# Kernel tuning notes

Hardware: AMD Instinct MI355X
Metric: run time of the kernel (lower is better)

## Reference

```python
import jax, jax.numpy as jnp
import numpy as np

ROWS, COLS, CH = 16, 16, 3
HID, HEADS, BLEN = 512, 8, 128
NUM_POINTS = ROWS * COLS            # 256
SEQ = ROWS * COLS * CH              # 768
NF = 256
L = 6
EPS = 1e-6


def setup_inputs() -> dict:
    key = jax.random.key(0)
    ks = jax.random.split(key, 16)
    w = 0.02  # keep logits in a sane range
    return {
        "X": jax.random.uniform(ks[0], (16, CH, ROWS, COLS), jnp.float32),
        "embed_table": jax.random.normal(ks[1], (NUM_POINTS * CH, HID), jnp.float32) * w,
        "Wq": jax.random.normal(ks[2], (L, HID, HID), jnp.float32) * w,
        "Wk": jax.random.normal(ks[3], (L, HID, HID), jnp.float32) * w,
        "Wv": jax.random.normal(ks[4], (L, HID, HID), jnp.float32) * w,
        "Wo": jax.random.normal(ks[5], (L, HID, HID), jnp.float32) * w,
        "ln1_g": jnp.ones((L, HID), jnp.float32),
        "ln1_b": jnp.zeros((L, HID), jnp.float32),
        "W1": jax.random.normal(ks[6], (L, HID, 4 * HID), jnp.float32) * w,
        "b1": jnp.zeros((L, 4 * HID), jnp.float32),
        "W2": jax.random.normal(ks[7], (L, 4 * HID, HID), jnp.float32) * w,
        "b2": jnp.zeros((L, HID), jnp.float32),
        "ln2_g": jnp.ones((L, HID), jnp.float32),
        "ln2_b": jnp.zeros((L, HID), jnp.float32),
        "proj_W": jax.random.normal(ks[8], (HID * SEQ, NF), jnp.float32) * w,
        "out_ln_g": jnp.ones((NF,), jnp.float32),
        "out_ln_b": jnp.zeros((NF,), jnp.float32),
    }


def _ln(x, g, b):
    m = jnp.mean(x, axis=-1, keepdims=True)
    v = jnp.mean(jnp.square(x - m), axis=-1, keepdims=True)
    return (x - m) * jax.lax.rsqrt(v + EPS) * g + b


def _timing_signal(x4):
    # x4: [B, ROWS, COLS*CH, HID]; 2 spatial dims
    nts = HID // 4
    inv = jnp.exp(jnp.arange(nts, dtype=jnp.float32) * (-np.log(10000.0) / (nts - 1)))
    def sig(length, prepad, postpad):
        pos = jnp.arange(length, dtype=jnp.float32)
        st = pos[:, None] * inv[None, :]
        s = jnp.concatenate([jnp.sin(st), jnp.cos(st)], axis=1)  # [len, 2*nts]
        return jnp.pad(s, ((0, 0), (prepad, postpad)))
    s0 = sig(x4.shape[1], 0, HID - 2 * nts)          # dim 0 (rows)
    s1 = sig(x4.shape[2], 2 * nts, 0)                # dim 1 (cols*ch)
    return x4 + s0[None, :, None, :] + s1[None, None, :, :]


def _local_attn(x, wq, wk, wv, wo):
    B, S, _ = x.shape
    dh = HID // HEADS
    def heads(w):
        return (x @ w).reshape(B, S, HEADS, dh).transpose(0, 2, 1, 3)
    q = heads(wq) * (dh ** -0.5)
    k = heads(wk)
    v = heads(wv)
    nb = S // BLEN  # S is a multiple of BLEN here (768/128=6), so no padding
    neg = jnp.float32(-1e9)
    bias1 = neg * jnp.triu(jnp.ones((BLEN, BLEN), jnp.float32), 1)
    logits1 = jnp.einsum('bhkd,bhqd->bhqk', k[:, :, :BLEN], q[:, :, :BLEN]) + bias1
    first = jax.nn.softmax(logits1, axis=-1) @ v[:, :, :BLEN]  # [B,H,BLEN,dh]
    qb = q.reshape(B, HEADS, nb, BLEN, dh)
    kb = k.reshape(B, HEADS, nb, BLEN, dh)
    vb = v.reshape(B, HEADS, nb, BLEN, dh)
    lk = jnp.concatenate([kb[:, :, :-1], kb[:, :, 1:]], axis=3)  # [B,H,nb-1,2B,dh]
    lv = jnp.concatenate([vb[:, :, :-1], vb[:, :, 1:]], axis=3)
    tq = qb[:, :, 1:]
    bias2 = neg * jnp.triu(jnp.ones((BLEN, 2 * BLEN), jnp.float32), BLEN + 1)
    logits2 = jnp.einsum('bhnkd,bhnqd->bhnqk', lk, tq) + bias2
    tail = jnp.einsum('bhnqk,bhnkd->bhnqd', jax.nn.softmax(logits2, axis=-1), lv)
    tail = tail.reshape(B, HEADS, (nb - 1) * BLEN, dh)
    out = jnp.concatenate([first, tail], axis=2)  # [B,H,S,dh]
    out = out.transpose(0, 2, 1, 3).reshape(B, S, HID)
    return out @ wo


def reference(X, embed_table, Wq, Wk, Wv, Wo, ln1_g, ln1_b, W1, b1, W2, b2,
              ln2_g, ln2_b, proj_W, out_ln_g, out_ln_b):
    B = X.shape[0]
    # [B,C,H,W] -> [B,H,W,C] -> [B,H,W*C]
    x = X.transpose(0, 2, 3, 1).reshape(B, ROWS, COLS * CH)
    idx = (x * (NUM_POINTS - 1)).astype(jnp.int32)
    chan_add = jnp.tile(jnp.arange(CH, dtype=jnp.int32) * NUM_POINTS, COLS)  # [W*C]
    idx = idx + chan_add[None, None, :]
    e = embed_table[idx] * (HID ** 0.5)             # [B,H,W*C,HID]
    # shift_and_pad over flattened spatial dims
    flat = e.reshape(B, SEQ, HID)
    flat = jnp.pad(flat[:, :-1], ((0, 0), (1, 0), (0, 0)))
    e = flat.reshape(B, ROWS, COLS * CH, HID)
    e = _timing_signal(e)
    h = e.reshape(B, SEQ, HID)
    for i in range(L):
        y = _local_attn(h, Wq[i], Wk[i], Wv[i], Wo[i])
        h = _ln(y + h, ln1_g[i], ln1_b[i])
        y = jax.nn.gelu(h @ W1[i] + b1[i], approximate=False) @ W2[i] + b2[i]
        h = _ln(y + h, ln2_g[i], ln2_b[i])
    out = h.reshape(B, SEQ * HID) @ proj_W
    out = jax.nn.gelu(out, approximate=False)
    return _ln(out, out_ln_g, out_ln_b)
```

## Files before the change

### kernel.cpp

```cpp
#include <hip/hip_runtime.h>
#include <cstddef>

typedef __bf16 bf16;
typedef bf16 bf16x4 __attribute__((ext_vector_type(4)));
typedef bf16 bf16x8 __attribute__((ext_vector_type(8)));
typedef float f32x4 __attribute__((ext_vector_type(4)));

#define NLAYER 6
#define HIDD 512
#define SEQL 768
#define NBATCH 16
#define MROWS 12288
#define QKVS 1536

__device__ __forceinline__ void gll16(const void* g, void* l) {
  __builtin_amdgcn_global_load_lds((const __attribute__((address_space(1))) void*)g,
                                   (__attribute__((address_space(3))) void*)l, 16, 0, 0);
}

__device__ __forceinline__ float gelu_f(float v) {
  return 0.5f * v * (1.0f + erff(v * 0.7071067811865475f));
}

#define VMC8 asm volatile("s_waitcnt vmcnt(8)" ::: "memory");
#define VMC4 asm volatile("s_waitcnt vmcnt(4)" ::: "memory");
#define VMC0 asm volatile("s_waitcnt vmcnt(0)" ::: "memory");

__global__ __launch_bounds__(256) void prep(
    const float* __restrict__ X, const float* __restrict__ ET,
    const float* __restrict__ Wq, const float* __restrict__ Wk,
    const float* __restrict__ Wv, const float* __restrict__ Wo,
    const float* __restrict__ W1, const float* __restrict__ W2,
    const float* __restrict__ ln1g, const float* __restrict__ ln1b,
    const float* __restrict__ ln2g, const float* __restrict__ ln2b,
    bf16* __restrict__ Wqkvt, bf16* __restrict__ Wot,
    bf16* __restrict__ W1t, bf16* __restrict__ W2t,
    float* __restrict__ vQg, float* __restrict__ vQb,
    float* __restrict__ vW1g, float* __restrict__ vW1b,
    bf16* __restrict__ Zg2) {
  const int bx = blockIdx.x;
  const int t = threadIdx.x;
  if (bx < 18432) {
    const int l = bx / 3072, idx = bx % 3072;
    const float* src;
    bf16* dst;
    int K, N, kb, nb;
    if (idx < 1024) {
      const int which = idx >> 8, tile = idx & 255;
      nb = (tile & 15) * 32; kb = (tile >> 4) * 32; K = 512; N = 512;
      const float* s4[4] = {Wq, Wk, Wv, Wo};
      src = s4[which] + (size_t)l * 512 * 512;
      dst = (which < 3) ? (Wqkvt + (size_t)l * QKVS * 512 + (size_t)which * 512 * 512)
                        : (Wot + (size_t)l * 512 * 512);
    } else if (idx < 2048) {
      const int local = idx - 1024;
      nb = (local & 63) * 32; kb = (local >> 6) * 32; K = 512; N = 2048;
      src = W1 + (size_t)l * 512 * 2048; dst = W1t + (size_t)l * 512 * 2048;
    } else {
      const int local = idx - 2048;
      nb = (local & 15) * 32; kb = (local >> 4) * 32; K = 2048; N = 512;
      src = W2 + (size_t)l * 2048 * 512; dst = W2t + (size_t)l * 2048 * 512;
    }
    __shared__ float tile[32 * 33];
#pragma unroll
    for (int i = 0; i < 4; ++i) {
      int lin = i * 256 + t, r = lin >> 5, c = lin & 31;
      tile[r * 33 + c] = src[(size_t)(kb + r) * N + nb + c];
    }
    __syncthreads();
#pragma unroll
    for (int i = 0; i < 4; ++i) {
      int lin = i * 256 + t, r = lin >> 5, c = lin & 31;
      dst[(size_t)(nb + r) * K + kb + c] = (bf16)tile[c * 33 + r];
    }
    return;
  }
  if (bx < 18432 + 84) {
    const int i = bx - 18432;
    const int l = i / 14;
    const int c = (i % 14) * 256 + t;
    if (c < 1536) {
      float gv = 0.f, bv = 0.f;
      if (l > 0) {
        const float* gin = ln2g + (l - 1) * 512;
        const float* bin = ln2b + (l - 1) * 512;
        const float* W;
        int cc = c;
        if (c < 512) { W = Wq + (size_t)l * 512 * 512; }
        else if (c < 1024) { W = Wk + (size_t)l * 512 * 512; cc = c - 512; }
        else { W = Wv + (size_t)l * 512 * 512; cc = c - 1024; }
        for (int k = 0; k < 512; ++k) {
          const float w = W[(size_t)k * 512 + cc];
          gv += gin[k] * w;
          bv += bin[k] * w;
        }
      }
      vQg[l * 1536 + c] = gv;
      vQb[l * 1536 + c] = bv;
    } else {
      const int cc = c - 1536;
      const float* g1 = ln1g + l * 512;
      const float* b1 = ln1b + l * 512;
      const float* W = W1 + (size_t)l * 512 * 2048;
      float gv = 0.f, bv = 0.f;
      for (int k = 0; k < 512; ++k) {
        const float w = W[(size_t)k * 2048 + cc];
        gv += g1[k] * w;
        bv += b1[k] * w;
      }
      vW1g[l * 2048 + cc] = gv;
      vW1b[l * 2048 + cc] = bv;
    }
    return;
  }
  const int bs = (bx - 18516) * 2 + (t >> 7);
  const int tl = t & 127;
  const int s = bs % SEQL;
  const int b = bs / SEQL;
  const int r = s / 48, c = s % 48;
  float vals[4] = {0.f, 0.f, 0.f, 0.f};
  const int ssrc = s - 1;
  if (ssrc >= 0) {
    const int rs = ssrc / 48, c48 = ssrc % 48;
    const int col = c48 / 3, ch = c48 % 3;
    const float x = X[((b * 3 + ch) * 16 + rs) * 16 + col];
    const int idx = (int)(x * 255.0f) + ch * 256;
    const float sq = 22.62741699796952f;
#pragma unroll
    for (int i = 0; i < 4; ++i) vals[i] = ET[(size_t)idx * HIDD + tl + 128 * i] * sq;
  }
  const float Cc = -0.07252236513366286f;
#pragma unroll
  for (int i = 0; i < 4; ++i) {
    const int d = tl + 128 * i;
    float ts;
    if (d < 128)      ts = sinf((float)r * expf((float)d * Cc));
    else if (d < 256) ts = cosf((float)r * expf((float)(d - 128) * Cc));
    else if (d < 384) ts = sinf((float)c * expf((float)(d - 256) * Cc));
    else              ts = cosf((float)c * expf((float)(d - 384) * Cc));
    Zg2[(size_t)bs * HIDD + d] = (bf16)(vals[i] + ts);
  }
}

template <int EPI, bool L0, int KT>
__global__ __launch_bounds__(256) void gemm2p(const bf16* __restrict__ A,
                                              const bf16* __restrict__ Bt,
                                              bf16* __restrict__ C,
                                              bf16* __restrict__ vT,
                                              const float* __restrict__ pIn,
                                              const float* __restrict__ vg,
                                              const float* __restrict__ vb,
                                              const float* __restrict__ bias,
                                              int N) {
  constexpr int K = KT;
  constexpr int NI = K >> 5;
  __shared__ char sbuf[49152];
  __shared__ float rsL[128], rsmL[128];
  const int tid = threadIdx.x;
  const int lane = tid & 63, w = tid >> 6;
  const int wr = w >> 1, wc = w & 1;
  const int l15 = lane & 15, g = lane >> 4;
  const int m0 = blockIdx.y * 128, n0 = blockIdx.x * 128;
  f32x4 acc[4][4] = {};
  const int rr0 = tid >> 2, kc = tid & 3;
  const bf16* Ap0 = A + (size_t)(m0 + rr0) * K + kc * 8;
  const bf16* Ap1 = A + (size_t)(m0 + 64 + rr0) * K + kc * 8;
  const bf16* Bp0 = Bt + (size_t)(n0 + rr0) * K + kc * 8;
  const bf16* Bp1 = Bt + (size_t)(n0 + 64 + rr0) * K + kc * 8;

  auto STAGE = [&](int st, int kt) {
    char* base = sbuf + st * 16384;
    gll16(Ap0 + kt, base + tid * 16);
    gll16(Ap1 + kt, base + 4096 + tid * 16);
    gll16(Bp0 + kt, base + 8192 + tid * 16);
    gll16(Bp1 + kt, base + 12288 + tid * 16);
  };

  STAGE(0, 0);
  STAGE(1, 32);
#pragma unroll 3
  for (int it = 0; it < NI; ++it) {
    const int cur = it % 3;
    if (it + 2 < NI) {
      STAGE((it + 2) % 3, (it + 2) * 32);
      VMC8;
    } else if (it + 1 < NI) {
      VMC4;
    } else {
      VMC0;
    }
    __builtin_amdgcn_s_barrier();
    const char* base = sbuf + cur * 16384;
    bf16x8 af[4], bv[4];
#pragma unroll
    for (int i = 0; i < 4; ++i)
      af[i] = *(const bf16x8*)(base + ((wr * 64 + i * 16 + l15) * 32 + 8 * g) * 2);
#pragma unroll
    for (int i = 0; i < 4; ++i)
      bv[i] = *(const bf16x8*)(base + 8192 + ((wc * 64 + i * 16 + l15) * 32 + 8 * g) * 2);
#pragma unroll
    for (int mi = 0; mi < 4; ++mi)
#pragma unroll
      for (int ni = 0; ni < 4; ++ni)
        acc[mi][ni] = __builtin_amdgcn_mfma_f32_16x16x32_bf16(af[mi], bv[ni], acc[mi][ni], 0, 0, 0);
    __builtin_amdgcn_s_barrier();
  }

  if constexpr (!L0) {
    if (tid < 128) {
      const int row = m0 + tid;
      float s = 0.f, q = 0.f;
#pragma unroll
      for (int j = 0; j < 8; ++j) {
        s += pIn[(size_t)j * MROWS + row];
        q += pIn[(size_t)(8 + j) * MROWS + row];
      }
      const float mean = s * (1.0f / 512.0f);
      const float var = q * (1.0f / 512.0f) - mean * mean;
      const float rs = rsqrtf(var + 1e-6f);
      rsL[tid] = rs;
      rsmL[tid] = rs * mean;
    }
    __syncthreads();
  }

  const bool VPATH = (EPI == 0) && (n0 >= 1024);
#pragma unroll
  for (int mi = 0; mi < 4; ++mi)
#pragma unroll
    for (int nf = 0; nf < 4; ++nf) {
      const int lr = wr * 64 + mi * 16 + 4 * g;
      const int row = m0 + lr;
      const int col = n0 + wc * 64 + nf * 16 + l15;
      float vgc = 0.f, vbc = 0.f, bc = 0.f;
      if constexpr (!L0) { vgc = vg[col]; vbc = vb[col]; }
      if constexpr (EPI == 1) bc = bias[col];
      float val[4];
#pragma unroll
      for (int r = 0; r < 4; ++r) {
        float a = acc[mi][nf][r];
        float v;
        if constexpr (L0) v = a;
        else v = rsL[lr + r] * a - rsmL[lr + r] * vgc + vbc;
        if constexpr (EPI == 1) v = gelu_f(v + bc);
        val[r] = v;
      }
      if (VPATH) {
        const int cv = col - 1024, hh = cv >> 6, dd = cv & 63;
        const int b = row / SEQL, s = row % SEQL;
        bf16x4 q4;
#pragma unroll
        for (int r = 0; r < 4; ++r) q4[r] = (bf16)val[r];
        *(bf16x4*)&vT[(size_t)((b * 8 + hh) * 64 + dd) * SEQL + s] = q4;
      } else {
#pragma unroll
        for (int r = 0; r < 4; ++r)
          C[(size_t)(row + r) * N + col] = (bf16)val[r];
      }
    }
}

template <int EPI, int KT>
__global__ __launch_bounds__(256) void gemm_fuse(const bf16* __restrict__ A,
                                                 const bf16* __restrict__ Bt,
                                                 const bf16* __restrict__ zgIn,
                                                 const float* __restrict__ pIn,
                                                 const float* __restrict__ vg_in,
                                                 const float* __restrict__ vb_in,
                                                 const float* __restrict__ extra_b,
                                                 const float* __restrict__ g_out,
                                                 bf16* __restrict__ zgOut,
                                                 float* __restrict__ pOut) {
  constexpr int N = 512;
  constexpr int K = KT;
  constexpr int NI = K >> 5;
  __shared__ char sbuf[49152];
  __shared__ float rsL[128], rsmL[128];
  const int tid = threadIdx.x;
  const int lane = tid & 63, w = tid >> 6;
  const int wr = w >> 1, wc = w & 1;
  const int l15 = lane & 15, g = lane >> 4;
  const int m0 = blockIdx.y * 128, n0 = blockIdx.x * 128;
  f32x4 acc[4][4] = {};
  const int rr0 = tid >> 2, kc = tid & 3;
  const bf16* Ap0 = A + (size_t)(m0 + rr0) * K + kc * 8;
  const bf16* Ap1 = A + (size_t)(m0 + 64 + rr0) * K + kc * 8;
  const bf16* Bp0 = Bt + (size_t)(n0 + rr0) * K + kc * 8;
  const bf16* Bp1 = Bt + (size_t)(n0 + 64 + rr0) * K + kc * 8;

  auto STAGE = [&](int st, int kt) {
    char* base = sbuf + st * 16384;
    gll16(Ap0 + kt, base + tid * 16);
    gll16(Ap1 + kt, base + 4096 + tid * 16);
    gll16(Bp0 + kt, base + 8192 + tid * 16);
    gll16(Bp1 + kt, base + 12288 + tid * 16);
  };

  STAGE(0, 0);
  STAGE(1, 32);
#pragma unroll 3
  for (int it = 0; it < NI; ++it) {
    const int cur = it % 3;
    if (it + 2 < NI) {
      STAGE((it + 2) % 3, (it + 2) * 32);
      VMC8;
    } else if (it + 1 < NI) {
      VMC4;
    } else {
      VMC0;
    }
    __builtin_amdgcn_s_barrier();
    const char* base = sbuf + cur * 16384;
    bf16x8 af[4], bv[4];
#pragma unroll
    for (int i = 0; i < 4; ++i)
      af[i] = *(const bf16x8*)(base + ((wr * 64 + i * 16 + l15) * 32 + 8 * g) * 2);
#pragma unroll
    for (int i = 0; i < 4; ++i)
      bv[i] = *(const bf16x8*)(base + 8192 + ((wc * 64 + i * 16 + l15) * 32 + 8 * g) * 2);
#pragma unroll
    for (int mi = 0; mi < 4; ++mi)
#pragma unroll
      for (int ni = 0; ni < 4; ++ni)
        acc[mi][ni] = __builtin_amdgcn_mfma_f32_16x16x32_bf16(af[mi], bv[ni], acc[mi][ni], 0, 0, 0);
    __builtin_amdgcn_s_barrier();
  }

  bf16* ztile = (bf16*)sbuf;
#pragma unroll
  for (int j = 0; j < 8; ++j) {
    const int row = j * 16 + (tid >> 4);
    const bf16* gsrc = zgIn + (size_t)(m0 + row) * N + n0 + (tid & 15) * 8;
    gll16(gsrc, sbuf + j * 4096 + tid * 16);
  }

  if constexpr (EPI != 0) {
    if (tid < 128) {
      const int row = m0 + tid;
      float s = 0.f, q = 0.f;
#pragma unroll
      for (int j = 0; j < 8; ++j) {
        s += pIn[(size_t)j * MROWS + row];
        q += pIn[(size_t)(8 + j) * MROWS + row];
      }
      const float mean = s * (1.0f / 512.0f);
      const float var = q * (1.0f / 512.0f) - mean * mean;
      const float rs = rsqrtf(var + 1e-6f);
      rsL[tid] = rs;
      rsmL[tid] = rs * mean;
    }
  }
  VMC0;
  __syncthreads();

  const int nb = n0 >> 7;
  float vgc[4], vbc[4], go[4], eb[4];
#pragma unroll
  for (int ni = 0; ni < 4; ++ni) {
    const int col = n0 + wc * 64 + ni * 16 + l15;
    if constexpr (EPI != 0) { vgc[ni] = vg_in[col]; vbc[ni] = vb_in[col]; }
    go[ni] = g_out[col];
    if constexpr (EPI == 2) eb[ni] = extra_b[col];
  }
#pragma unroll
  for (int mi = 0; mi < 4; ++mi) {
#pragma unroll
    for (int rr = 0; rr < 4; ++rr) {
      const int lr = wr * 64 + mi * 16 + 4 * g + rr;
      const int row = m0 + lr;
      float s = 0.f, q = 0.f;
#pragma unroll
      for (int ni = 0; ni < 4; ++ni) {
        const int lc = wc * 64 + ni * 16 + l15;
        const float zgv = (float)ztile[lr * 128 + lc];
        float hprev;
        if constexpr (EPI == 0) hprev = zgv;
        else hprev = rsL[lr] * zgv - rsmL[lr] * vgc[ni] + vbc[ni];
        float z = acc[mi][ni][rr] + hprev;
        if constexpr (EPI == 2) z += eb[ni];
        s += z;
        q += z * z;
        ztile[lr * 128 + lc] = (bf16)(z * go[ni]);
      }
      s += __shfl_xor(s, 1); s += __shfl_xor(s, 2); s += __shfl_xor(s, 4); s += __shfl_xor(s, 8);
      q += __shfl_xor(q, 1); q += __shfl_xor(q, 2); q += __shfl_xor(q, 4); q += __shfl_xor(q, 8);
      if (l15 == 0) {
        pOut[(size_t)(nb * 2 + wc) * MROWS + row] = s;
        pOut[(size_t)(8 + nb * 2 + wc) * MROWS + row] = q;
      }
    }
  }
  __syncthreads();
#pragma unroll
  for (int i = 0; i < 8; ++i) {
    const int id = i * 256 + tid;
    const int row = id >> 4, c16 = id & 15;
    bf16x8 v = *(const bf16x8*)&ztile[row * 128 + c16 * 8];
    *(bf16x8*)&zgOut[(size_t)(m0 + row) * N + n0 + c16 * 8] = v;
  }
}

template <int NKEY>
__device__ __forceinline__ void attn_body(int n, int h, int b,
                                          const bf16* __restrict__ Qb,
                                          const bf16* __restrict__ Kb,
                                          const bf16* __restrict__ Vt,
                                          bf16* __restrict__ O,
                                          bf16* __restrict__ Ks,
                                          bf16* __restrict__ Vs,
                                          bf16* __restrict__ Pc) {
  constexpr int NF = NKEY / 16;
  constexpr int KC = NKEY / 32;
  constexpr int VG = NKEY / 8;
  const int tid = threadIdx.x, w = tid >> 6, lane = tid & 63;
  const int l15 = lane & 15, g = lane >> 4;
  const int keybase = (NKEY == 128) ? 0 : (n - 1) * 128;
  const int qbase = n * 128;

#pragma unroll
  for (int p = 0; p < NKEY / 64; ++p) {
    const int j = p * 512 + tid;
    const int row = j >> 3, lg = j & 7;
    const int pg = lg ^ (row & 7);
    gll16(Kb + (size_t)(b * SEQL + keybase + row) * QKVS + h * 64 + pg * 8, Ks + j * 8);
  }
#pragma unroll
  for (int p = 0; p < NKEY / 64; ++p) {
    const int j = p * 512 + tid;
    const int row = j / VG, lg = j % VG;
    const int pg = lg ^ (row & (VG - 1));
    gll16(Vt + (size_t)((b * 8 + h) * 64 + row) * SEQL + keybase + pg * 8, Vs + j * 8);
  }

  const bf16* qrow = Qb + (size_t)(b * SEQL + qbase + w * 16 + l15) * QKVS + h * 64;
  bf16x8 qf0 = *(const bf16x8*)(qrow + 8 * g);
  bf16x8 qf1 = *(const bf16x8*)(qrow + 32 + 8 * g);

  VMC0;
  __syncthreads();

  f32x4 S[NF];
#pragma unroll
  for (int nf = 0; nf < NF; ++nf) S[nf] = f32x4{0.f, 0.f, 0.f, 0.f};
#pragma unroll
  for (int nf = 0; nf < NF; ++nf) {
    const int krow = nf * 16 + l15;
    const int pg0 = g ^ (krow & 7);
    const int pg1 = (g + 4) ^ (krow & 7);
    bf16x8 kf0 = *(const bf16x8*)&Ks[krow * 64 + pg0 * 8];
    bf16x8 kf1 = *(const bf16x8*)&Ks[krow * 64 + pg1 * 8];
    S[nf] = __builtin_amdgcn_mfma_f32_16x16x32_bf16(qf0, kf0, S[nf], 0, 0, 0);
    S[nf] = __builtin_amdgcn_mfma_f32_16x16x32_bf16(qf1, kf1, S[nf], 0, 0, 0);
  }
#pragma unroll
  for (int rr = 0; rr < 4; ++rr) {
    const int qloc = w * 16 + 4 * g + rr;
    float mx = -3.0e38f;
#pragma unroll
    for (int nf = 0; nf < NF; ++nf) {
      const int key = nf * 16 + l15;
      const bool valid = (NKEY == 128) ? (key <= qloc) : (key <= qloc + 128);
      float v = valid ? S[nf][rr] * 0.125f : -1.0e9f;
      S[nf][rr] = v;
      mx = fmaxf(mx, v);
    }
    mx = fmaxf(mx, __shfl_xor(mx, 1));
    mx = fmaxf(mx, __shfl_xor(mx, 2));
    mx = fmaxf(mx, __shfl_xor(mx, 4));
    mx = fmaxf(mx, __shfl_xor(mx, 8));
    float sden = 0.f;
#pragma unroll
    for (int nf = 0; nf < NF; ++nf) {
      float e = expf(S[nf][rr] - mx);
      S[nf][rr] = e;
      sden += e;
    }
    sden += __shfl_xor(sden, 1);
    sden += __shfl_xor(sden, 2);
    sden += __shfl_xor(sden, 4);
    sden += __shfl_xor(sden, 8);
    const float rcp = 1.0f / sden;
#pragma unroll
    for (int nf = 0; nf < NF; ++nf) S[nf][rr] *= rcp;
  }

  bf16* pcw = Pc + w * 640;
  f32x4 Oacc[4];
#pragma unroll
  for (int i = 0; i < 4; ++i) Oacc[i] = f32x4{0.f, 0.f, 0.f, 0.f};
#pragma unroll
  for (int kc = 0; kc < KC; ++kc) {
#pragma unroll
    for (int rr = 0; rr < 4; ++rr) {
      pcw[(4 * g + rr) * 40 + l15] = (bf16)S[2 * kc][rr];
      pcw[(4 * g + rr) * 40 + 16 + l15] = (bf16)S[2 * kc + 1][rr];
    }
    bf16x8 pa = *(const bf16x8*)&pcw[l15 * 40 + 8 * g];
#pragma unroll
    for (int nf = 0; nf < 4; ++nf) {
      const int vrow = nf * 16 + l15;
      const int pg = (kc * 4 + g) ^ (vrow & (VG - 1));
      bf16x8 vf = *(const bf16x8*)&Vs[vrow * NKEY + pg * 8];
      Oacc[nf] = __builtin_amdgcn_mfma_f32_16x16x32_bf16(pa, vf, Oacc[nf], 0, 0, 0);
    }
  }
#pragma unroll
  for (int nf = 0; nf < 4; ++nf)
#pragma unroll
    for (int rr = 0; rr < 4; ++rr)
      O[(size_t)(b * SEQL + qbase + w * 16 + 4 * g + rr) * HIDD + h * 64 + nf * 16 + l15] =
          (bf16)Oacc[nf][rr];
}

__global__ __launch_bounds__(512, 4) void attn_all(const bf16* __restrict__ Qb,
                                                   const bf16* __restrict__ Kb,
                                                   const bf16* __restrict__ Vt,
                                                   bf16* __restrict__ O) {
  __shared__ bf16 Ks[256 * 64];
  __shared__ bf16 Vs[64 * 256];
  __shared__ bf16 Pc[8 * 640];
  const int n = blockIdx.x, h = blockIdx.y, b = blockIdx.z;
  if (n == 0)
    attn_body<128>(0, h, b, Qb, Kb, Vt, O, Ks, Vs, Pc);
  else
    attn_body<256>(n, h, b, Qb, Kb, Vt, O, Ks, Vs, Pc);
}

__global__ __launch_bounds__(256) void proj_partial(const bf16* __restrict__ zg2,
                                                    const float* __restrict__ pSQ2,
                                                    const float* __restrict__ g5,
                                                    const float* __restrict__ b5,
                                                    const float* __restrict__ W,
                                                    float* __restrict__ part) {
  const int kc = blockIdx.x;
  const int t = threadIdx.x;
  __shared__ float Al[512 * 20];
  __shared__ float gld[512], bld[512], rsP[16], rsmP[16];
  gld[t] = g5[t]; gld[t + 256] = g5[t + 256];
  bld[t] = b5[t]; bld[t + 256] = b5[t + 256];
  if (t < 16) {
    const int row = t * SEQL + kc;
    float s = 0.f, q = 0.f;
#pragma unroll
    for (int j = 0; j < 8; ++j) {
      s += pSQ2[(size_t)j * MROWS + row];
      q += pSQ2[(size_t)(8 + j) * MROWS + row];
    }
    const float mean = s * (1.0f / 512.0f);
    const float var = q * (1.0f / 512.0f) - mean * mean;
    const float rs = rsqrtf(var + 1e-6f);
    rsP[t] = rs;
    rsmP[t] = rs * mean;
  }
  __syncthreads();
#pragma unroll
  for (int i = 0; i < 32; ++i) {
    int lin = i * 256 + t, m = lin >> 9, kk = lin & 511;
    const int row = m * SEQL + kc;
    Al[kk * 20 + m] = rsP[m] * (float)zg2[(size_t)row * 512 + kk] - rsmP[m] * gld[kk] + bld[kk];
  }
  __syncthreads();
  const size_t k0 = (size_t)kc * 512;
  float acc[16] = {};
  for (int kk = 0; kk < 512; ++kk) {
    const float wv = W[(k0 + kk) * 256 + t];
    const f32x4* a = (const f32x4*)&Al[kk * 20];
#pragma unroll
    for (int j = 0; j < 4; ++j) {
      f32x4 av = a[j];
      acc[j * 4 + 0] += av[0] * wv;
      acc[j * 4 + 1] += av[1] * wv;
      acc[j * 4 + 2] += av[2] * wv;
      acc[j * 4 + 3] += av[3] * wv;
    }
  }
#pragma unroll
  for (int m = 0; m < 16; ++m) part[(size_t)kc * 4096 + m * 256 + t] = acc[m];
}

__global__ __launch_bounds__(256) void proj_reduce1(const float* __restrict__ part,
                                                    float* __restrict__ part2) {
  const int i = blockIdx.x * 256 + threadIdx.x;
  const int cb = blockIdx.y;
  float s = 0.f;
  for (int c = cb * 64; c < cb * 64 + 64; ++c) s += part[(size_t)c * 4096 + i];
  part2[(size_t)cb * 4096 + i] = s;
}

__global__ __launch_bounds__(256) void proj_final(const float* __restrict__ part2,
                                                  const float* __restrict__ g,
                                                  const float* __restrict__ bt,
                                                  float* __restrict__ out) {
  const int row = blockIdx.x, t = threadIdx.x;
  float v = 0.f;
#pragma unroll
  for (int c = 0; c < 12; ++c) v += part2[(size_t)c * 4096 + row * 256 + t];
  const float x = gelu_f(v);
  __shared__ float red[256];
  red[t] = x;
  __syncthreads();
  for (int off = 128; off > 0; off >>= 1) {
    if (t < off) red[t] += red[t + off];
    __syncthreads();
  }
  const float mean = red[0] * (1.0f / 256.0f);
  __syncthreads();
  const float dx = x - mean;
  red[t] = dx * dx;
  __syncthreads();
  for (int off = 128; off > 0; off >>= 1) {
    if (t < off) red[t] += red[t + off];
    __syncthreads();
  }
  const float var = red[0] * (1.0f / 256.0f);
  const float rs = rsqrtf(var + 1e-6f);
  out[row * 256 + t] = dx * rs * g[t] + bt[t];
}

extern "C" void kernel_launch(void* const* d_in, const int* in_sizes, int n_in,
                              void* d_out, int out_size, void* d_ws, size_t ws_size,
                              hipStream_t stream) {
  const float* X = (const float*)d_in[0];
  const float* ET = (const float*)d_in[1];
  const float* Wq = (const float*)d_in[2];
  const float* Wk = (const float*)d_in[3];
  const float* Wv = (const float*)d_in[4];
  const float* Wo = (const float*)d_in[5];
  const float* ln1g = (const float*)d_in[6];
  const float* ln1b = (const float*)d_in[7];
  const float* W1 = (const float*)d_in[8];
  const float* b1 = (const float*)d_in[9];
  const float* W2 = (const float*)d_in[10];
  const float* b2 = (const float*)d_in[11];
  const float* ln2g = (const float*)d_in[12];
  const float* ln2b = (const float*)d_in[13];
  const float* PW = (const float*)d_in[14];
  const float* og = (const float*)d_in[15];
  const float* obv = (const float*)d_in[16];
  float* out = (float*)d_out;

  char* p = (char*)d_ws;
  auto alloc = [&](size_t bytes) {
    char* r = p;
    p += (bytes + 255) & ~(size_t)255;
    return r;
  };
  bf16* Wqkvt = (bf16*)alloc((size_t)NLAYER * QKVS * 512 * 2);
  bf16* Wot = (bf16*)alloc((size_t)NLAYER * 512 * 512 * 2);
  bf16* W1t = (bf16*)alloc((size_t)NLAYER * 512 * 2048 * 2);
  bf16* W2t = (bf16*)alloc((size_t)NLAYER * 512 * 2048 * 2);
  float* vQg = (float*)alloc((size_t)NLAYER * QKVS * 4);
  float* vQb = (float*)alloc((size_t)NLAYER * QKVS * 4);
  float* vW1g = (float*)alloc((size_t)NLAYER * 2048 * 4);
  float* vW1b = (float*)alloc((size_t)NLAYER * 2048 * 4);
  bf16* zg2 = (bf16*)alloc((size_t)MROWS * HIDD * 2);
  bf16* zg1 = (bf16*)alloc((size_t)MROWS * HIDD * 2);
  float* pSQ1 = (float*)alloc((size_t)16 * MROWS * 4);
  float* pSQ2 = (float*)alloc((size_t)16 * MROWS * 4);
  bf16* qkvB = (bf16*)alloc((size_t)MROWS * QKVS * 2);
  bf16* vT = (bf16*)alloc((size_t)MROWS * HIDD * 2);
  bf16* aO = (bf16*)alloc((size_t)MROWS * HIDD * 2);
  bf16* mid = (bf16*)alloc((size_t)MROWS * 2048 * 2);
  float* part = (float*)alloc((size_t)768 * 4096 * 4);
  float* part2 = (float*)alloc((size_t)12 * 4096 * 4);
  (void)ws_size; (void)n_in; (void)in_sizes; (void)out_size;

  prep<<<24660, 256, 0, stream>>>(X, ET, Wq, Wk, Wv, Wo, W1, W2, ln1g, ln1b, ln2g, ln2b,
                                  Wqkvt, Wot, W1t, W2t, vQg, vQb, vW1g, vW1b, zg2);

  for (int i = 0; i < NLAYER; ++i) {
    const bf16* WqkvL = Wqkvt + (size_t)i * QKVS * 512;
    const bf16* WoL = Wot + (size_t)i * 512 * 512;
    const bf16* W1L = W1t + (size_t)i * 512 * 2048;
    const bf16* W2L = W2t + (size_t)i * 512 * 2048;
    if (i == 0)
      gemm2p<0, true, 512><<<dim3(12, 96), 256, 0, stream>>>(zg2, WqkvL, qkvB, vT, pSQ2,
                                                             vQg, vQb, nullptr, QKVS);
    else
      gemm2p<0, false, 512><<<dim3(12, 96), 256, 0, stream>>>(zg2, WqkvL, qkvB, vT, pSQ2,
                                                              vQg + i * QKVS, vQb + i * QKVS,
                                                              nullptr, QKVS);
    attn_all<<<dim3(6, 8, 16), 512, 0, stream>>>(qkvB, qkvB + 512, vT, aO);
    if (i == 0)
      gemm_fuse<0, 512><<<dim3(4, 96), 256, 0, stream>>>(aO, WoL, zg2, nullptr, nullptr,
                                                         nullptr, nullptr, ln1g, zg1, pSQ1);
    else
      gemm_fuse<1, 512><<<dim3(4, 96), 256, 0, stream>>>(aO, WoL, zg2, pSQ2,
                                                         ln2g + (i - 1) * 512,
                                                         ln2b + (i - 1) * 512, nullptr,
                                                         ln1g + i * 512, zg1, pSQ1);
    gemm2p<1, false, 512><<<dim3(16, 96), 256, 0, stream>>>(zg1, W1L, mid, nullptr, pSQ1,
                                                            vW1g + i * 2048, vW1b + i * 2048,
                                                            b1 + i * 2048, 2048);
    gemm_fuse<2, 2048><<<dim3(4, 96), 256, 0, stream>>>(mid, W2L, zg1, pSQ1, ln1g + i * 512,
                                                        ln1b + i * 512, b2 + i * 512,
                                                        ln2g + i * 512, zg2, pSQ2);
  }

  proj_partial<<<768, 256, 0, stream>>>(zg2, pSQ2, ln2g + 5 * 512, ln2b + 5 * 512, PW, part);
  proj_reduce1<<<dim3(16, 12), 256, 0, stream>>>(part, part2);
  proj_final<<<16, 256, 0, stream>>>(part2, og, obv, out);
}
```

Baseline: 1.246 ms.

## Widen GEMM tiles to 128x256 and merge projection reduction into one tail kernel

All fused GEMM kernels now use 128x256 output tiles. Each wave computes 64x128 with more MFMAs per LDS fragment load, the LDS staging buffers are larger, and launch bounds request 2 blocks per CU. The per-row LayerNorm partial sums shrink from 8 to 4 slots to match the wider tiles. The two-stage projection reduction is replaced by one kernel in which 16 blocks each serially sum 768 partials. This trades a launch for much less parallel reduction. The larger tiles raise register pressure and halve the grid size (e.g. 192 blocks for the Wo/W2 GEMMs), which could hurt occupancy and load balance.

```diff
diff --git a/kernel.cpp b/kernel.cpp
--- a/kernel.cpp
+++ b/kernel.cpp
@@ -22,8 +22,8 @@
   return 0.5f * v * (1.0f + erff(v * 0.7071067811865475f));
 }
 
-#define VMC8 asm volatile("s_waitcnt vmcnt(8)" ::: "memory");
-#define VMC4 asm volatile("s_waitcnt vmcnt(4)" ::: "memory");
+#define VMC12 asm volatile("s_waitcnt vmcnt(12)" ::: "memory");
+#define VMC6 asm volatile("s_waitcnt vmcnt(6)" ::: "memory");
 #define VMC0 asm volatile("s_waitcnt vmcnt(0)" ::: "memory");
 
 __global__ __launch_bounds__(256) void prep(
@@ -143,37 +143,40 @@
 }
 
 template <int EPI, bool L0, int KT>
-__global__ __launch_bounds__(256) void gemm2p(const bf16* __restrict__ A,
-                                              const bf16* __restrict__ Bt,
-                                              bf16* __restrict__ C,
-                                              bf16* __restrict__ vT,
-                                              const float* __restrict__ pIn,
-                                              const float* __restrict__ vg,
-                                              const float* __restrict__ vb,
-                                              const float* __restrict__ bias,
-                                              int N) {
+__global__ __launch_bounds__(256, 2) void gemm2p(const bf16* __restrict__ A,
+                                                 const bf16* __restrict__ Bt,
+                                                 bf16* __restrict__ C,
+                                                 bf16* __restrict__ vT,
+                                                 const float* __restrict__ pIn,
+                                                 const float* __restrict__ vg,
+                                                 const float* __restrict__ vb,
+                                                 const float* __restrict__ bias,
+                                                 int N) {
   constexpr int K = KT;
   constexpr int NI = K >> 5;
-  __shared__ char sbuf[49152];
+  __shared__ char sbuf[73728];
   __shared__ float rsL[128], rsmL[128];
   const int tid = threadIdx.x;
   const int lane = tid & 63, w = tid >> 6;
-  const int wr = w >> 1, wc = w & 1;
+  const int wm = w >> 1, wn = w & 1;
   const int l15 = lane & 15, g = lane >> 4;
-  const int m0 = blockIdx.y * 128, n0 = blockIdx.x * 128;
-  f32x4 acc[4][4] = {};
-  const int rr0 = tid >> 2, kc = tid & 3;
-  const bf16* Ap0 = A + (size_t)(m0 + rr0) * K + kc * 8;
-  const bf16* Ap1 = A + (size_t)(m0 + 64 + rr0) * K + kc * 8;
-  const bf16* Bp0 = Bt + (size_t)(n0 + rr0) * K + kc * 8;
-  const bf16* Bp1 = Bt + (size_t)(n0 + 64 + rr0) * K + kc * 8;
+  const int m0 = blockIdx.y * 128, n0 = blockIdx.x * 256;
+  f32x4 acc[4][8] = {};
 
   auto STAGE = [&](int st, int kt) {
-    char* base = sbuf + st * 16384;
-    gll16(Ap0 + kt, base + tid * 16);
-    gll16(Ap1 + kt, base + 4096 + tid * 16);
-    gll16(Bp0 + kt, base + 8192 + tid * 16);
-    gll16(Bp1 + kt, base + 12288 + tid * 16);
+    char* base = sbuf + st * 24576;
+#pragma unroll
+    for (int j = 0; j < 2; ++j) {
+      const int idx = j * 256 + tid;
+      const int row = idx >> 2, gc = idx & 3;
+      gll16(A + (size_t)(m0 + row) * K + kt + gc * 8, base + idx * 16);
+    }
+#pragma unroll
+    for (int j = 0; j < 4; ++j) {
+      const int idx = j * 256 + tid;
+      const int row = idx >> 2, gc = idx & 3;
+      gll16(Bt + (size_t)(n0 + row) * K + kt + gc * 8, base + 8192 + idx * 16);
+    }
   };
 
   STAGE(0, 0);
@@ -183,25 +186,25 @@
     const int cur = it % 3;
     if (it + 2 < NI) {
       STAGE((it + 2) % 3, (it + 2) * 32);
-      VMC8;
+      VMC12;
     } else if (it + 1 < NI) {
-      VMC4;
+      VMC6;
     } else {
       VMC0;
     }
     __builtin_amdgcn_s_barrier();
-    const char* base = sbuf + cur * 16384;
-    bf16x8 af[4], bv[4];
+    const char* base = sbuf + cur * 24576;
+    bf16x8 af[4], bv[8];
 #pragma unroll
     for (int i = 0; i < 4; ++i)
-      af[i] = *(const bf16x8*)(base + ((wr * 64 + i * 16 + l15) * 32 + 8 * g) * 2);
-#pragma unroll
-    for (int i = 0; i < 4; ++i)
-      bv[i] = *(const bf16x8*)(base + 8192 + ((wc * 64 + i * 16 + l15) * 32 + 8 * g) * 2);
+      af[i] = *(const bf16x8*)(base + ((wm * 64 + i * 16 + l15) * 32 + 8 * g) * 2);
+#pragma unroll
+    for (int i = 0; i < 8; ++i)
+      bv[i] = *(const bf16x8*)(base + 8192 + ((wn * 128 + i * 16 + l15) * 32 + 8 * g) * 2);
 #pragma unroll
     for (int mi = 0; mi < 4; ++mi)
 #pragma unroll
-      for (int ni = 0; ni < 4; ++ni)
+      for (int ni = 0; ni < 8; ++ni)
         acc[mi][ni] = __builtin_amdgcn_mfma_f32_16x16x32_bf16(af[mi], bv[ni], acc[mi][ni], 0, 0, 0);
     __builtin_amdgcn_s_barrier();
   }
@@ -211,9 +214,9 @@
       const int row = m0 + tid;
       float s = 0.f, q = 0.f;
 #pragma unroll
-      for (int j = 0; j < 8; ++j) {
+      for (int j = 0; j < 4; ++j) {
         s += pIn[(size_t)j * MROWS + row];
-        q += pIn[(size_t)(8 + j) * MROWS + row];
+        q += pIn[(size_t)(4 + j) * MROWS + row];
       }
       const float mean = s * (1.0f / 512.0f);
       const float var = q * (1.0f / 512.0f) - mean * mean;
@@ -228,10 +231,10 @@
 #pragma unroll
   for (int mi = 0; mi < 4; ++mi)
 #pragma unroll
-    for (int nf = 0; nf < 4; ++nf) {
-      const int lr = wr * 64 + mi * 16 + 4 * g;
+    for (int nf = 0; nf < 8; ++nf) {
+      const int lr = wm * 64 + mi * 16 + 4 * g;
       const int row = m0 + lr;
-      const int col = n0 + wc * 64 + nf * 16 + l15;
+      const int col = n0 + wn * 128 + nf * 16 + l15;
       float vgc = 0.f, vbc = 0.f, bc = 0.f;
       if constexpr (!L0) { vgc = vg[col]; vbc = vb[col]; }
       if constexpr (EPI == 1) bc = bias[col];
@@ -261,39 +264,42 @@
 }
 
 template <int EPI, int KT>
-__global__ __launch_bounds__(256) void gemm_fuse(const bf16* __restrict__ A,
-                                                 const bf16* __restrict__ Bt,
-                                                 const bf16* __restrict__ zgIn,
-                                                 const float* __restrict__ pIn,
-                                                 const float* __restrict__ vg_in,
-                                                 const float* __restrict__ vb_in,
-                                                 const float* __restrict__ extra_b,
-                                                 const float* __restrict__ g_out,
-                                                 bf16* __restrict__ zgOut,
-                                                 float* __restrict__ pOut) {
+__global__ __launch_bounds__(256, 2) void gemm_fuse(const bf16* __restrict__ A,
+                                                    const bf16* __restrict__ Bt,
+                                                    const bf16* __restrict__ zgIn,
+                                                    const float* __restrict__ pIn,
+                                                    const float* __restrict__ vg_in,
+                                                    const float* __restrict__ vb_in,
+                                                    const float* __restrict__ extra_b,
+                                                    const float* __restrict__ g_out,
+                                                    bf16* __restrict__ zgOut,
+                                                    float* __restrict__ pOut) {
   constexpr int N = 512;
   constexpr int K = KT;
   constexpr int NI = K >> 5;
-  __shared__ char sbuf[49152];
+  __shared__ char sbuf[73728];
   __shared__ float rsL[128], rsmL[128];
   const int tid = threadIdx.x;
   const int lane = tid & 63, w = tid >> 6;
-  const int wr = w >> 1, wc = w & 1;
+  const int wm = w >> 1, wn = w & 1;
   const int l15 = lane & 15, g = lane >> 4;
-  const int m0 = blockIdx.y * 128, n0 = blockIdx.x * 128;
-  f32x4 acc[4][4] = {};
-  const int rr0 = tid >> 2, kc = tid & 3;
-  const bf16* Ap0 = A + (size_t)(m0 + rr0) * K + kc * 8;
-  const bf16* Ap1 = A + (size_t)(m0 + 64 + rr0) * K + kc * 8;
-  const bf16* Bp0 = Bt + (size_t)(n0 + rr0) * K + kc * 8;
-  const bf16* Bp1 = Bt + (size_t)(n0 + 64 + rr0) * K + kc * 8;
+  const int m0 = blockIdx.y * 128, n0 = blockIdx.x * 256;
+  f32x4 acc[4][8] = {};
 
   auto STAGE = [&](int st, int kt) {
-    char* base = sbuf + st * 16384;
-    gll16(Ap0 + kt, base + tid * 16);
-    gll16(Ap1 + kt, base + 4096 + tid * 16);
-    gll16(Bp0 + kt, base + 8192 + tid * 16);
-    gll16(Bp1 + kt, base + 12288 + tid * 16);
+    char* base = sbuf + st * 24576;
+#pragma unroll
+    for (int j = 0; j < 2; ++j) {
+      const int idx = j * 256 + tid;
+      const int row = idx >> 2, gc = idx & 3;
+      gll16(A + (size_t)(m0 + row) * K + kt + gc * 8, base + idx * 16);
+    }
+#pragma unroll
+    for (int j = 0; j < 4; ++j) {
+      const int idx = j * 256 + tid;
+      const int row = idx >> 2, gc = idx & 3;
+      gll16(Bt + (size_t)(n0 + row) * K + kt + gc * 8, base + 8192 + idx * 16);
+    }
   };
 
   STAGE(0, 0);
@@ -303,35 +309,35 @@
     const int cur = it % 3;
     if (it + 2 < NI) {
       STAGE((it + 2) % 3, (it + 2) * 32);
-      VMC8;
+      VMC12;
     } else if (it + 1 < NI) {
-      VMC4;
+      VMC6;
     } else {
       VMC0;
     }
     __builtin_amdgcn_s_barrier();
-    const char* base = sbuf + cur * 16384;
-    bf16x8 af[4], bv[4];
+    const char* base = sbuf + cur * 24576;
+    bf16x8 af[4], bv[8];
 #pragma unroll
     for (int i = 0; i < 4; ++i)
-      af[i] = *(const bf16x8*)(base + ((wr * 64 + i * 16 + l15) * 32 + 8 * g) * 2);
-#pragma unroll
-    for (int i = 0; i < 4; ++i)
-      bv[i] = *(const bf16x8*)(base + 8192 + ((wc * 64 + i * 16 + l15) * 32 + 8 * g) * 2);
+      af[i] = *(const bf16x8*)(base + ((wm * 64 + i * 16 + l15) * 32 + 8 * g) * 2);
+#pragma unroll
+    for (int i = 0; i < 8; ++i)
+      bv[i] = *(const bf16x8*)(base + 8192 + ((wn * 128 + i * 16 + l15) * 32 + 8 * g) * 2);
 #pragma unroll
     for (int mi = 0; mi < 4; ++mi)
 #pragma unroll
-      for (int ni = 0; ni < 4; ++ni)
+      for (int ni = 0; ni < 8; ++ni)
         acc[mi][ni] = __builtin_amdgcn_mfma_f32_16x16x32_bf16(af[mi], bv[ni], acc[mi][ni], 0, 0, 0);
     __builtin_amdgcn_s_barrier();
   }
 
   bf16* ztile = (bf16*)sbuf;
 #pragma unroll
-  for (int j = 0; j < 8; ++j) {
-    const int row = j * 16 + (tid >> 4);
-    const bf16* gsrc = zgIn + (size_t)(m0 + row) * N + n0 + (tid & 15) * 8;
-    gll16(gsrc, sbuf + j * 4096 + tid * 16);
+  for (int j = 0; j < 16; ++j) {
+    const int idx = j * 256 + tid;
+    const int row = idx >> 5, gc = idx & 31;
+    gll16(zgIn + (size_t)(m0 + row) * N + n0 + gc * 8, sbuf + idx * 16);
   }
 
   if constexpr (EPI != 0) {
@@ -339,9 +345,9 @@
       const int row = m0 + tid;
       float s = 0.f, q = 0.f;
 #pragma unroll
-      for (int j = 0; j < 8; ++j) {
+      for (int j = 0; j < 4; ++j) {
         s += pIn[(size_t)j * MROWS + row];
-        q += pIn[(size_t)(8 + j) * MROWS + row];
+        q += pIn[(size_t)(4 + j) * MROWS + row];
       }
       const float mean = s * (1.0f / 512.0f);
       const float var = q * (1.0f / 512.0f) - mean * mean;
@@ -353,11 +359,11 @@
   VMC0;
   __syncthreads();
 
-  const int nb = n0 >> 7;
-  float vgc[4], vbc[4], go[4], eb[4];
-#pragma unroll
-  for (int ni = 0; ni < 4; ++ni) {
-    const int col = n0 + wc * 64 + ni * 16 + l15;
+  const int nb = n0 >> 8;
+  float vgc[8], vbc[8], go[8], eb[8];
+#pragma unroll
+  for (int ni = 0; ni < 8; ++ni) {
+    const int col = n0 + wn * 128 + ni * 16 + l15;
     if constexpr (EPI != 0) { vgc[ni] = vg_in[col]; vbc[ni] = vb_in[col]; }
     go[ni] = g_out[col];
     if constexpr (EPI == 2) eb[ni] = extra_b[col];
@@ -366,13 +372,13 @@
   for (int mi = 0; mi < 4; ++mi) {
 #pragma unroll
     for (int rr = 0; rr < 4; ++rr) {
-      const int lr = wr * 64 + mi * 16 + 4 * g + rr;
+      const int lr = wm * 64 + mi * 16 + 4 * g + rr;
       const int row = m0 + lr;
       float s = 0.f, q = 0.f;
 #pragma unroll
-      for (int ni = 0; ni < 4; ++ni) {
-        const int lc = wc * 64 + ni * 16 + l15;
-        const float zgv = (float)ztile[lr * 128 + lc];
+      for (int ni = 0; ni < 8; ++ni) {
+        const int lc = wn * 128 + ni * 16 + l15;
+        const float zgv = (float)ztile[lr * 256 + lc];
         float hprev;
         if constexpr (EPI == 0) hprev = zgv;
         else hprev = rsL[lr] * zgv - rsmL[lr] * vgc[ni] + vbc[ni];
@@ -380,22 +386,22 @@
         if constexpr (EPI == 2) z += eb[ni];
         s += z;
         q += z * z;
-        ztile[lr * 128 + lc] = (bf16)(z * go[ni]);
+        ztile[lr * 256 + lc] = (bf16)(z * go[ni]);
       }
       s += __shfl_xor(s, 1); s += __shfl_xor(s, 2); s += __shfl_xor(s, 4); s += __shfl_xor(s, 8);
       q += __shfl_xor(q, 1); q += __shfl_xor(q, 2); q += __shfl_xor(q, 4); q += __shfl_xor(q, 8);
       if (l15 == 0) {
-        pOut[(size_t)(nb * 2 + wc) * MROWS + row] = s;
-        pOut[(size_t)(8 + nb * 2 + wc) * MROWS + row] = q;
-      }
-    }
-  }
-  __syncthreads();
-#pragma unroll
-  for (int i = 0; i < 8; ++i) {
+        pOut[(size_t)(nb * 2 + wn) * MROWS + row] = s;
+        pOut[(size_t)(4 + nb * 2 + wn) * MROWS + row] = q;
+      }
+    }
+  }
+  __syncthreads();
+#pragma unroll
+  for (int i = 0; i < 16; ++i) {
     const int id = i * 256 + tid;
-    const int row = id >> 4, c16 = id & 15;
-    bf16x8 v = *(const bf16x8*)&ztile[row * 128 + c16 * 8];
+    const int row = id >> 5, c16 = id & 31;
+    bf16x8 v = *(const bf16x8*)&ztile[row * 256 + c16 * 8];
     *(bf16x8*)&zgOut[(size_t)(m0 + row) * N + n0 + c16 * 8] = v;
   }
 }
@@ -542,9 +548,9 @@
     const int row = t * SEQL + kc;
     float s = 0.f, q = 0.f;
 #pragma unroll
-    for (int j = 0; j < 8; ++j) {
+    for (int j = 0; j < 4; ++j) {
       s += pSQ2[(size_t)j * MROWS + row];
-      q += pSQ2[(size_t)(8 + j) * MROWS + row];
+      q += pSQ2[(size_t)(4 + j) * MROWS + row];
     }
     const float mean = s * (1.0f / 512.0f);
     const float var = q * (1.0f / 512.0f) - mean * mean;
@@ -578,23 +584,13 @@
   for (int m = 0; m < 16; ++m) part[(size_t)kc * 4096 + m * 256 + t] = acc[m];
 }
 
-__global__ __launch_bounds__(256) void proj_reduce1(const float* __restrict__ part,
-                                                    float* __restrict__ part2) {
-  const int i = blockIdx.x * 256 + threadIdx.x;
-  const int cb = blockIdx.y;
-  float s = 0.f;
-  for (int c = cb * 64; c < cb * 64 + 64; ++c) s += part[(size_t)c * 4096 + i];
-  part2[(size_t)cb * 4096 + i] = s;
-}
-
-__global__ __launch_bounds__(256) void proj_final(const float* __restrict__ part2,
-                                                  const float* __restrict__ g,
-                                                  const float* __restrict__ bt,
-                                                  float* __restrict__ out) {
+__global__ __launch_bounds__(256) void proj_tail(const float* __restrict__ part,
+                                                 const float* __restrict__ g,
+                                                 const float* __restrict__ bt,
+                                                 float* __restrict__ out) {
   const int row = blockIdx.x, t = threadIdx.x;
   float v = 0.f;
-#pragma unroll
-  for (int c = 0; c < 12; ++c) v += part2[(size_t)c * 4096 + row * 256 + t];
+  for (int c = 0; c < 768; ++c) v += part[(size_t)c * 4096 + row * 256 + t];
   const float x = gelu_f(v);
   __shared__ float red[256];
   red[t] = x;
@@ -655,14 +651,13 @@
   float* vW1b = (float*)alloc((size_t)NLAYER * 2048 * 4);
   bf16* zg2 = (bf16*)alloc((size_t)MROWS * HIDD * 2);
   bf16* zg1 = (bf16*)alloc((size_t)MROWS * HIDD * 2);
-  float* pSQ1 = (float*)alloc((size_t)16 * MROWS * 4);
-  float* pSQ2 = (float*)alloc((size_t)16 * MROWS * 4);
+  float* pSQ1 = (float*)alloc((size_t)8 * MROWS * 4);
+  float* pSQ2 = (float*)alloc((size_t)8 * MROWS * 4);
   bf16* qkvB = (bf16*)alloc((size_t)MROWS * QKVS * 2);
   bf16* vT = (bf16*)alloc((size_t)MROWS * HIDD * 2);
   bf16* aO = (bf16*)alloc((size_t)MROWS * HIDD * 2);
   bf16* mid = (bf16*)alloc((size_t)MROWS * 2048 * 2);
   float* part = (float*)alloc((size_t)768 * 4096 * 4);
-  float* part2 = (float*)alloc((size_t)12 * 4096 * 4);
   (void)ws_size; (void)n_in; (void)in_sizes; (void)out_size;
 
   prep<<<24660, 256, 0, stream>>>(X, ET, Wq, Wk, Wv, Wo, W1, W2, ln1g, ln1b, ln2g, ln2b,
@@ -674,30 +669,29 @@
     const bf16* W1L = W1t + (size_t)i * 512 * 2048;
     const bf16* W2L = W2t + (size_t)i * 512 * 2048;
     if (i == 0)
-      gemm2p<0, true, 512><<<dim3(12, 96), 256, 0, stream>>>(zg2, WqkvL, qkvB, vT, pSQ2,
-                                                             vQg, vQb, nullptr, QKVS);
+      gemm2p<0, true, 512><<<dim3(6, 96), 256, 0, stream>>>(zg2, WqkvL, qkvB, vT, pSQ2,
+                                                            vQg, vQb, nullptr, QKVS);
     else
-      gemm2p<0, false, 512><<<dim3(12, 96), 256, 0, stream>>>(zg2, WqkvL, qkvB, vT, pSQ2,
-                                                              vQg + i * QKVS, vQb + i * QKVS,
-                                                              nullptr, QKVS);
+      gemm2p<0, false, 512><<<dim3(6, 96), 256, 0, stream>>>(zg2, WqkvL, qkvB, vT, pSQ2,
+                                                             vQg + i * QKVS, vQb + i * QKVS,
+                                                             nullptr, QKVS);
     attn_all<<<dim3(6, 8, 16), 512, 0, stream>>>(qkvB, qkvB + 512, vT, aO);
     if (i == 0)
-      gemm_fuse<0, 512><<<dim3(4, 96), 256, 0, stream>>>(aO, WoL, zg2, nullptr, nullptr,
+      gemm_fuse<0, 512><<<dim3(2, 96), 256, 0, stream>>>(aO, WoL, zg2, nullptr, nullptr,
                                                          nullptr, nullptr, ln1g, zg1, pSQ1);
     else
-      gemm_fuse<1, 512><<<dim3(4, 96), 256, 0, stream>>>(aO, WoL, zg2, pSQ2,
+      gemm_fuse<1, 512><<<dim3(2, 96), 256, 0, stream>>>(aO, WoL, zg2, pSQ2,
                                                          ln2g + (i - 1) * 512,
                                                          ln2b + (i - 1) * 512, nullptr,
                                                          ln1g + i * 512, zg1, pSQ1);
-    gemm2p<1, false, 512><<<dim3(16, 96), 256, 0, stream>>>(zg1, W1L, mid, nullptr, pSQ1,
-                                                            vW1g + i * 2048, vW1b + i * 2048,
-                                                            b1 + i * 2048, 2048);
-    gemm_fuse<2, 2048><<<dim3(4, 96), 256, 0, stream>>>(mid, W2L, zg1, pSQ1, ln1g + i * 512,
+    gemm2p<1, false, 512><<<dim3(8, 96), 256, 0, stream>>>(zg1, W1L, mid, nullptr, pSQ1,
+                                                           vW1g + i * 2048, vW1b + i * 2048,
+                                                           b1 + i * 2048, 2048);
+    gemm_fuse<2, 2048><<<dim3(2, 96), 256, 0, stream>>>(mid, W2L, zg1, pSQ1, ln1g + i * 512,
                                                         ln1b + i * 512, b2 + i * 512,
                                                         ln2g + i * 512, zg2, pSQ2);
   }
 
   proj_partial<<<768, 256, 0, stream>>>(zg2, pSQ2, ln2g + 5 * 512, ln2b + 5 * 512, PW, part);
-  proj_reduce1<<<dim3(16, 12), 256, 0, stream>>>(part, part2);
-  proj_final<<<16, 256, 0, stream>>>(part2, og, obv, out);
-}
+  proj_tail<<<16, 256, 0, stream>>>(part, og, obv, out);
+}
```

Result: slower. 1.445 ms (+16.0%).
